# Kernel tuning notes

Measured on AMD Instinct MI355X. Metric: run time of the kernel, lower is better.

Reference implementation:

```python
import jax, jax.numpy as jnp
import numpy as np

D_MODEL = 1024
N_HEADS = 16
D_K = D_MODEL // N_HEADS
LN_EPS = 1e-5
NEG = -1e9


def setup_inputs() -> dict:
    key = jax.random.key(0)
    ks = jax.random.split(key, 12)
    B, S = 4, 2048
    s = 1.0 / np.sqrt(D_MODEL)
    # causal mask (1 = keep, 0 = masked)
    causal = jnp.tril(jnp.ones((S, S), dtype=jnp.int32))
    mask = jnp.broadcast_to(causal[None, None], (B, 1, S, S))
    return {
        "Q": jax.random.normal(ks[0], (B, S, D_MODEL), jnp.float32),
        "K": jax.random.normal(ks[1], (B, S, D_MODEL), jnp.float32),
        "V": jax.random.normal(ks[2], (B, S, D_MODEL), jnp.float32),
        "mask": mask,
        "Wq": jax.random.normal(ks[3], (D_MODEL, D_MODEL), jnp.float32) * s,
        "bq": jnp.zeros((D_MODEL,), jnp.float32),
        "Wk": jax.random.normal(ks[4], (D_MODEL, D_MODEL), jnp.float32) * s,
        "bk": jnp.zeros((D_MODEL,), jnp.float32),
        "Wv": jax.random.normal(ks[5], (D_MODEL, D_MODEL), jnp.float32) * s,
        "bv": jnp.zeros((D_MODEL,), jnp.float32),
        "Wo": jax.random.normal(ks[6], (D_MODEL, D_MODEL), jnp.float32) * s,
        "bo": jnp.zeros((D_MODEL,), jnp.float32),
        "ln_gamma": jnp.ones((D_MODEL,), jnp.float32),
        "ln_beta": jnp.zeros((D_MODEL,), jnp.float32),
    }


def _split_heads(x, B, S):
    # (B,S,D) -> (B,H,S,d_k)
    return x.reshape(B, S, N_HEADS, D_K).transpose(0, 2, 1, 3)


def reference(Q, K, V, mask, Wq, bq, Wk, bk, Wv, bv, Wo, bo, ln_gamma, ln_beta):
    B, S, _ = Q.shape
    residual = Q
    q = _split_heads(Q @ Wq + bq, B, S)
    k = _split_heads(K @ Wk + bk, B, S)
    v = _split_heads(V @ Wv + bv, B, S)
    scores = jnp.einsum("bhqd,bhkd->bhqk", q, k) / np.sqrt(D_K).astype(np.float32)
    scores = jnp.where(mask == 0, jnp.float32(NEG), scores)
    attn = jax.nn.softmax(scores, axis=-1)  # dropout p=0 -> identity
    ctx = jnp.einsum("bhqk,bhkd->bhqd", attn, v)
    ctx = ctx.transpose(0, 2, 1, 3).reshape(B, S, D_MODEL)
    out = ctx @ Wo + bo
    x = out + residual
    mu = jnp.mean(x, axis=-1, keepdims=True)
    var = jnp.mean(jnp.square(x - mu), axis=-1, keepdims=True)
    y = (x - mu) * jax.lax.rsqrt(var + LN_EPS) * ln_gamma + ln_beta
    return (y, attn)
```

## Files before the change

### kernel.cpp

```cpp
#include <hip/hip_runtime.h>

#define D_MODEL 1024
#define NH 16
#define DKH 64
#define SEQ 2048
#define BATCH 4
#define ROWS (BATCH*SEQ)

typedef _Float16 f16;
typedef _Float16 f16x4 __attribute__((ext_vector_type(4)));
typedef _Float16 f16x8 __attribute__((ext_vector_type(8)));
typedef float f32x4 __attribute__((ext_vector_type(4)));

#define MFMA16(a,b,c) __builtin_amdgcn_mfma_f32_16x16x32_f16((a),(b),(c),0,0,0)
#define CFENCE() asm volatile("" ::: "memory")

__device__ __forceinline__ void gload16(const void* g, void* l) {
  __builtin_amdgcn_global_load_lds((const __attribute__((address_space(1))) void*)g,
                                   (__attribute__((address_space(3))) void*)l,
                                   16, 0, 0);
}


__global__ __launch_bounds__(256) void cvt_w_kernel(const float* __restrict__ Wq,
    const float* __restrict__ Wk, const float* __restrict__ Wv, const float* __restrict__ Wo,
    f16* __restrict__ dst)
{
  const float* W = (blockIdx.z==0)?Wq:(blockIdx.z==1)?Wk:(blockIdx.z==2)?Wv:Wo;
  f16* d = dst + (size_t)blockIdx.z * ((size_t)D_MODEL*D_MODEL);
  int idx = blockIdx.x*256 + threadIdx.x;
  int k = idx>>10, n = idx&1023;
  d[(size_t)n*D_MODEL + k] = (f16)W[idx];
}


template<int AF32>
__global__ __launch_bounds__(256) void gemm128(
    const void* __restrict__ A0, const void* __restrict__ A1, const void* __restrict__ A2,
    const f16* __restrict__ WTbase,
    const float* __restrict__ bias0, const float* __restrict__ bias1, const float* __restrict__ bias2,
    f16* __restrict__ out0, f16* __restrict__ out1, f16* __restrict__ out2,
    const float* __restrict__ resid, float* __restrict__ xout, int modeBase)
{
  __shared__ f16 Al[2][128*32];
  __shared__ f16 Bl[2][128*32];
  const int t = threadIdx.x, w = t>>6, l = t&63;
  const int nwg = (int)gridDim.x;
  const int wg = ((int)blockIdx.x & 7) * (nwg >> 3) + ((int)blockIdx.x >> 3);
  const int z  = wg >> 9;
  const int r2 = wg & 511;
  const int bm = r2 >> 3, bn = r2 & 7;
  const int mode = modeBase + z;
  const f16* WT = WTbase + (size_t)mode * ((size_t)D_MODEL*D_MODEL);
  const float* bias = (mode==0)?bias0:(mode==1)?bias1:(mode==2)?bias2:bias0;
  const int wm = w>>1, wn = w&1;
  const int lr = l>>2, lc = l&3, fr = l&15, fg = l>>4;
  f32x4 acc[4][4] = {};
  const char* Bb = (const char*)(WT + (size_t)bn*128*D_MODEL);

#define STAGEB(bufv, ktv) do { \
    char* Bd = (char*)&Bl[0][0] + (bufv)*8192; \
    _Pragma("unroll") \
    for (int cc=0; cc<2; ++cc) { \
      int r0 = w*32 + cc*16; \
      gload16(Bb + (size_t)(r0+lr)*2048 + (ktv)*64 + lc*16, Bd + r0*64); \
    } \
  } while(0)

#define COMPUTEK(bufv) do { \
    const f16* Ac = (const f16*)((char*)&Al[0][0] + (bufv)*8192); \
    const f16* Bc = (const f16*)((char*)&Bl[0][0] + (bufv)*8192); \
    f16x8 a[4], b[4]; \
    _Pragma("unroll") \
    for (int i=0;i<4;++i) a[i] = *(const f16x8*)(Ac + (wm*64+i*16+fr)*32 + fg*8); \
    _Pragma("unroll") \
    for (int j=0;j<4;++j) b[j] = *(const f16x8*)(Bc + (wn*64+j*16+fr)*32 + fg*8); \
    _Pragma("unroll") \
    for (int i=0;i<4;++i) \
      _Pragma("unroll") \
      for (int j=0;j<4;++j) \
        acc[i][j] = MFMA16(a[i], b[j], acc[i][j]); \
  } while(0)

#define LOADA_TO(dst, ktv) do { \
    _Pragma("unroll") \
    for (int s=0;s<2;++s) \
      _Pragma("unroll") \
      for (int q=0;q<2;++q) \
        dst[s][q] = *(const f32x4*)(Arow + (size_t)s*16*1024 + (ktv)*32 + q*4); \
  } while(0)

#define WRITEA_FROM(src, bufv) do { \
    char* Ad = (char*)&Al[0][0] + (bufv)*8192 + w*2048 + l*16; \
    _Pragma("unroll") \
    for (int s=0;s<2;++s) { \
      f16x8 pk; \
      _Pragma("unroll") \
      for (int q=0;q<2;++q) \
        _Pragma("unroll") \
        for (int m2=0;m2<4;++m2) pk[q*4+m2] = (f16)src[s][q][m2]; \
      *(f16x8*)(Ad + s*1024) = pk; \
    } \
  } while(0)

#define BAR_FENCED() do { __builtin_amdgcn_s_barrier(); CFENCE(); } while(0)

  if constexpr (AF32) {
    const float* A32 = (const float*)((z==0)?A0:(z==1)?A1:A2);
    const float* Arow = A32 + (size_t)(bm*128 + w*32 + (l>>2))*1024 + (l&3)*8;
    f32x4 laA[2][2], laB[2][2];
    LOADA_TO(laA, 0);
    STAGEB(0, 0);
    WRITEA_FROM(laA, 0);
    LOADA_TO(laB, 1);
    CFENCE();
    for (int kt2=0; kt2<30; kt2+=2) {
      STAGEB((kt2+1)&1, kt2+1);
      LOADA_TO(laA, kt2+2);
      asm volatile("s_waitcnt vmcnt(6) lgkmcnt(0)" ::: "memory");
      BAR_FENCED();
      COMPUTEK(kt2&1);
      WRITEA_FROM(laB, (kt2+1)&1);
      CFENCE();
      BAR_FENCED();
      STAGEB((kt2+2)&1, kt2+2);
      LOADA_TO(laB, kt2+3);
      asm volatile("s_waitcnt vmcnt(6) lgkmcnt(0)" ::: "memory");
      BAR_FENCED();
      COMPUTEK((kt2+1)&1);
      WRITEA_FROM(laA, (kt2+2)&1);
      CFENCE();
      BAR_FENCED();
    }
    STAGEB(1, 31);
    asm volatile("s_waitcnt vmcnt(6) lgkmcnt(0)" ::: "memory");
    BAR_FENCED();
    COMPUTEK(0);
    WRITEA_FROM(laB, 1);
    CFENCE();
    BAR_FENCED();
    asm volatile("s_waitcnt vmcnt(0) lgkmcnt(0)" ::: "memory");
    BAR_FENCED();
    COMPUTEK(1);
  } else {
    const char* Ab = (const char*)((const f16*)A0 + (size_t)bm*128*D_MODEL);
    auto STAGEA = [&](int bufv, int ktv) {
      char* Ad = (char*)&Al[0][0] + bufv*8192;
      #pragma unroll
      for (int cc=0; cc<2; ++cc) {
        int r0 = w*32 + cc*16;
        gload16(Ab + (size_t)(r0+lr)*2048 + ktv*64 + lc*16, Ad + r0*64);
      }
    };
    STAGEA(0,0); STAGEB(0, 0);
    CFENCE();
    for (int kt=0; kt<31; ++kt) {
      const int cur = kt & 1;
      STAGEA(cur^1, kt+1);
      STAGEB(cur^1, kt+1);
      asm volatile("s_waitcnt vmcnt(4)" ::: "memory");
      BAR_FENCED();
      COMPUTEK(cur);
      CFENCE();
      BAR_FENCED();
    }
    asm volatile("s_waitcnt vmcnt(0)" ::: "memory");
    BAR_FENCED();
    COMPUTEK(1);
  }

#undef STAGEB
#undef COMPUTEK
#undef LOADA_TO
#undef WRITEA_FROM
#undef BAR_FENCED

  #pragma unroll
  for (int j=0;j<4;++j) {
    int col = bn*128 + wn*64 + j*16 + fr;
    float bz = bias[col];
    #pragma unroll
    for (int i=0;i<4;++i) {
      int row0 = bm*128 + wm*64 + i*16 + fg*4;
      f32x4 v = acc[i][j];
      if (mode==0) {
        int hh = col>>6, dk = col&63;
        #pragma unroll
        for (int r=0;r<4;++r) {
          int row = row0+r; int b_ = row>>11, s = row&(SEQ-1);
          out0[((size_t)(b_*NH+hh)*SEQ + s)*DKH + dk] = (f16)((v[r]+bz)*0.125f);
        }
      } else if (mode==1) {
        int hh = col>>6, dk = col&63;
        #pragma unroll
        for (int r=0;r<4;++r) {
          int row = row0+r; int b_ = row>>11, s = row&(SEQ-1);
          out1[((size_t)(b_*NH+hh)*SEQ + s)*DKH + dk] = (f16)(v[r]+bz);
        }
      } else if (mode==2) {
        int hh = col>>6, dk = col&63;
        int b_ = row0>>11, s0 = row0&(SEQ-1);
        f16x4 pk;
        #pragma unroll
        for (int r=0;r<4;++r) pk[r] = (f16)(v[r]+bz);
        *(f16x4*)(out2 + ((size_t)(b_*NH+hh)*DKH + dk)*SEQ + s0) = pk;
      } else {
        #pragma unroll
        for (int r=0;r<4;++r) {
          size_t o = (size_t)(row0+r)*D_MODEL + col;
          xout[o] = v[r] + bz + resid[o];
        }
      }
    }
  }
}


__global__ __launch_bounds__(256) void attn_kernel(
    const f16* __restrict__ qws, const f16* __restrict__ kws, const f16* __restrict__ vTws,
    float* __restrict__ attn, f16* __restrict__ ctx)
{
  __shared__ f16 el[4][32*128];
  const int t = threadIdx.x, w = t>>6, l = t&63;
  const int wg = ((int)blockIdx.x & 7)*64 + ((int)blockIdx.x >> 3);
  const int bh = wg >> 3;
  const int pr = wg & 7;
  const int qtA = pr, qtB = 15 - pr;
  const int fr = l & 15, fg = l >> 4;
  const f16* kp = kws + (size_t)bh*SEQ*DKH;
  const f16* vp = vTws + (size_t)bh*DKH*SEQ;
  const f16* qpA = qws + ((size_t)bh*SEQ + (size_t)qtA*128)*DKH;
  const f16* qpB = qws + ((size_t)bh*SEQ + (size_t)qtB*128)*DKH;
  float* apA = attn + ((size_t)bh*SEQ + (size_t)qtA*128)*SEQ;
  float* apB = attn + ((size_t)bh*SEQ + (size_t)qtB*128)*SEQ;
  f16* elw = (f16*)&el[w][0];
  const int swzx = (fr & 7) << 2;
  const int rbrow = l >> 5;
  const int rbslot = l & 31;

  f16x8 qfA[2][2], qfB[2][2];
  #pragma unroll
  for (int i=0;i<2;++i)
    #pragma unroll
    for (int kc=0;kc<2;++kc) {
      qfA[i][kc] = *(const f16x8*)(qpA + (w*32 + i*16 + fr)*DKH + kc*32 + fg*8);
      qfB[i][kc] = *(const f16x8*)(qpB + (w*32 + i*16 + fr)*DKH + kc*32 + fg*8);
    }

  auto fill_tile = [&](float* apr, int kt2) {
    f32x4 z4 = {0.f,0.f,0.f,0.f};
    #pragma unroll
    for (int i2=0;i2<16;++i2) {
      int idx = t + i2*256;
      int row = idx >> 5, c4 = idx & 31;
      __builtin_nontemporal_store(z4, (f32x4*)(apr + (size_t)row*SEQ + (size_t)kt2*128 + c4*4));
    }
  };
  const int cB = pr;

  float psumA[2] = {0.f,0.f}, psumB[2] = {0.f,0.f};
  int u = 0, f = 0;
  const int np1 = qtB + 1;
  auto drip_fills = [&]() {
    while (f*np1 < u*15) {
      if (f < cB) fill_tile(apB, qtB+1+f);
      else        fill_tile(apA, qtA+1+(f-cB));
      ++f;
    }
  };

  for (int kt=0; kt<=qtA; ++kt) {
    const f16* kb = kp + (size_t)kt*128*DKH;
    const bool diagA = (kt == qtA);
    #pragma unroll
    for (int jh=0; jh<2; ++jh) {
      f32x4 scB[2][4] = {};
      f32x4 scA[2][4] = {};
      #pragma unroll
      for (int j2=0;j2<4;++j2) {
        const int j = jh*4 + j2;
        #pragma unroll
        for (int kc=0;kc<2;++kc) {
          f16x8 kf = *(const f16x8*)(kb + (j*16+fr)*DKH + kc*32 + fg*8);
          scB[0][j2] = MFMA16(kf, qfB[0][kc], scB[0][j2]);
          scB[1][j2] = MFMA16(kf, qfB[1][kc], scB[1][j2]);
          scA[0][j2] = MFMA16(kf, qfA[0][kc], scA[0][j2]);
          scA[1][j2] = MFMA16(kf, qfA[1][kc], scA[1][j2]);
        }
      }
      #pragma unroll
      for (int i=0;i<2;++i)
        #pragma unroll
        for (int j2=0;j2<4;++j2)
          #pragma unroll
          for (int r=0;r<4;++r) psumB[i] += __expf(scB[i][j2][r]);
      if (diagA) {
        #pragma unroll
        for (int i=0;i<2;++i) {
          int rloc = w*32 + i*16 + fr;
          #pragma unroll
          for (int j2=0;j2<4;++j2)
            #pragma unroll
            for (int r=0;r<4;++r) {
              int cloc = (jh*4+j2)*16 + fg*4 + r;
              if (cloc <= rloc) psumA[i] += __expf(scA[i][j2][r]);
            }
        }
      } else {
        #pragma unroll
        for (int i=0;i<2;++i)
          #pragma unroll
          for (int j2=0;j2<4;++j2)
            #pragma unroll
            for (int r=0;r<4;++r) psumA[i] += __expf(scA[i][j2][r]);
      }
    }
    ++u; drip_fills();
  }

  for (int kt=qtA+1; kt<=qtB; ++kt) {
    const f16* kb = kp + (size_t)kt*128*DKH;
    const bool diagB = (kt == qtB);
    #pragma unroll
    for (int jh=0; jh<2; ++jh) {
      f32x4 sc[2][4] = {};
      #pragma unroll
      for (int j2=0;j2<4;++j2) {
        const int j = jh*4 + j2;
        #pragma unroll
        for (int kc=0;kc<2;++kc) {
          f16x8 kf = *(const f16x8*)(kb + (j*16+fr)*DKH + kc*32 + fg*8);
          sc[0][j2] = MFMA16(kf, qfB[0][kc], sc[0][j2]);
          sc[1][j2] = MFMA16(kf, qfB[1][kc], sc[1][j2]);
        }
      }
      if (diagB) {
        #pragma unroll
        for (int i=0;i<2;++i) {
          int rloc = w*32 + i*16 + fr;
          #pragma unroll
          for (int j2=0;j2<4;++j2)
            #pragma unroll
            for (int r=0;r<4;++r) {
              int cloc = (jh*4+j2)*16 + fg*4 + r;
              if (cloc <= rloc) psumB[i] += __expf(sc[i][j2][r]);
            }
        }
      } else {
        #pragma unroll
        for (int i=0;i<2;++i)
          #pragma unroll
          for (int j2=0;j2<4;++j2)
            #pragma unroll
            for (int r=0;r<4;++r) psumB[i] += __expf(sc[i][j2][r]);
      }
    }
    ++u; drip_fills();
  }

  #pragma unroll
  for (int m=16; m<64; m<<=1) {
    psumA[0] += __shfl_xor(psumA[0], m, 64);
    psumA[1] += __shfl_xor(psumA[1], m, 64);
    psumB[0] += __shfl_xor(psumB[0], m, 64);
    psumB[1] += __shfl_xor(psumB[1], m, 64);
  }
  float rinvA[2] = {1.f/psumA[0], 1.f/psumA[1]};
  float rinvB[2] = {1.f/psumB[0], 1.f/psumB[1]};

  f32x4 av[2][4];
  auto pass2_tile = [&](int ktv, bool diag, const f16x8 (&qf)[2][2], const float (&rinv)[2], float* apr) {
    const f16* kb = kp + (size_t)ktv*128*DKH;
    #pragma unroll
    for (int jh=0; jh<2; ++jh) {
      f32x4 sc[2][4] = {};
      __builtin_amdgcn_s_setprio(1);
      #pragma unroll
      for (int j2=0;j2<4;++j2) {
        const int j = jh*4 + j2;
        #pragma unroll
        for (int kc=0;kc<2;++kc) {
          f16x8 kf = *(const f16x8*)(kb + (j*16+fr)*DKH + kc*32 + fg*8);
          sc[0][j2] = MFMA16(kf, qf[0][kc], sc[0][j2]);
          sc[1][j2] = MFMA16(kf, qf[1][kc], sc[1][j2]);
        }
      }
      __builtin_amdgcn_s_setprio(0);
      #pragma unroll
      for (int i=0;i<2;++i) {
        const int rloc = w*32 + i*16 + fr;
        #pragma unroll
        for (int j2=0;j2<4;++j2) {
          const int j = jh*4 + j2;
          f16x4 ef;
          #pragma unroll
          for (int r=0;r<4;++r) {
            int cloc = j*16 + fg*4 + r;
            float e = (diag && cloc > rloc) ? 0.f : __expf(sc[i][j2][r]) * rinv[i];
            ef[r] = (f16)e;
          }
          *(f16x4*)(elw + (i*16+fr)*128 + (((j*4+fg) ^ swzx) << 2)) = ef;
        }
      }
    }
    {
      float* apk = apr + (size_t)(w*32)*SEQ + (size_t)ktv*128;
      #pragma unroll
      for (int p=0;p<16;++p) {
        int row = p*2 + rbrow;
        f16x4 pv4 = *(const f16x4*)(elw + row*128 + ((rbslot ^ ((row&7)<<2)) << 2));
        f32x4 o4; o4[0]=(float)pv4[0]; o4[1]=(float)pv4[1]; o4[2]=(float)pv4[2]; o4[3]=(float)pv4[3];
        __builtin_nontemporal_store(o4, (f32x4*)(apk + (size_t)row*SEQ + rbslot*4));
      }
    }
    __builtin_amdgcn_s_setprio(1);
    #pragma unroll
    for (int c=0;c<4;++c) {
      f16x8 pf0 = *(const f16x8*)(elw + (fr)*128    + (((c*8+fg*2) ^ swzx) << 2));
      f16x8 pf1 = *(const f16x8*)(elw + (16+fr)*128 + (((c*8+fg*2) ^ swzx) << 2));
      #pragma unroll
      for (int j2=0;j2<4;++j2) {
        f16x8 vf = *(const f16x8*)(vp + (j2*16+fr)*SEQ + ktv*128 + c*32 + fg*8);
        av[0][j2] = MFMA16(vf, pf0, av[0][j2]);
        av[1][j2] = MFMA16(vf, pf1, av[1][j2]);
      }
    }
    __builtin_amdgcn_s_setprio(0);
  };
  auto ctx_store = [&](int qtv) {
    const int b_ = bh >> 4, hh = bh & 15;
    #pragma unroll
    for (int i=0;i<2;++i) {
      size_t rowoff = ((size_t)b_*SEQ + (size_t)qtv*128 + w*32 + i*16 + fr) * D_MODEL + hh*DKH;
      #pragma unroll
      for (int j2=0;j2<4;++j2) {
        f16x4 pk;
        #pragma unroll
        for (int r=0;r<4;++r) pk[r] = (f16)av[i][j2][r];
        *(f16x4*)(ctx + rowoff + j2*16 + fg*4) = pk;
      }
    }
  };

  #pragma unroll
  for (int i=0;i<2;++i)
    #pragma unroll
    for (int j2=0;j2<4;++j2) av[i][j2] = (f32x4){0.f,0.f,0.f,0.f};
  for (int kt=0; kt<=qtA; ++kt) pass2_tile(kt, kt==qtA, qfA, rinvA, apA);
  ctx_store(qtA);

  #pragma unroll
  for (int i=0;i<2;++i)
    #pragma unroll
    for (int j2=0;j2<4;++j2) av[i][j2] = (f32x4){0.f,0.f,0.f,0.f};
  for (int kt=0; kt<=qtB; ++kt) pass2_tile(kt, kt==qtB, qfB, rinvB, apB);
  ctx_store(qtB);
}


__global__ __launch_bounds__(256) void ln_kernel(const float* __restrict__ x,
    const float* __restrict__ gamma, const float* __restrict__ beta, float* __restrict__ y)
{
  __shared__ float red[4];
  __shared__ float red2[4];
  const int t = threadIdx.x, w = t>>6, l = t&63;
  const size_t row = blockIdx.x;
  float4 v = ((const float4*)(x + row*D_MODEL))[t];
  float s = v.x+v.y+v.z+v.w;
  #pragma unroll
  for (int m=1;m<64;m<<=1) s += __shfl_xor(s, m, 64);
  if (l==0) red[w] = s;
  __syncthreads();
  float mu = (red[0]+red[1]+red[2]+red[3]) * (1.f/D_MODEL);
  float dx=v.x-mu, dy=v.y-mu, dz=v.z-mu, dw=v.w-mu;
  float q = dx*dx+dy*dy+dz*dz+dw*dw;
  #pragma unroll
  for (int m=1;m<64;m<<=1) q += __shfl_xor(q, m, 64);
  if (l==0) red2[w] = q;
  __syncthreads();
  float var = (red2[0]+red2[1]+red2[2]+red2[3]) * (1.f/D_MODEL);
  float rs = rsqrtf(var + 1e-5f);
  float4 g  = ((const float4*)gamma)[t];
  float4 bb = ((const float4*)beta)[t];
  float4 o;
  o.x = dx*rs*g.x + bb.x;
  o.y = dy*rs*g.y + bb.y;
  o.z = dz*rs*g.z + bb.z;
  o.w = dw*rs*g.w + bb.w;
  ((float4*)(y + row*D_MODEL))[t] = o;
}


extern "C" void kernel_launch(void* const* d_in, const int* in_sizes, int n_in,
                              void* d_out, int out_size, void* d_ws, size_t ws_size,
                              hipStream_t stream)
{
  const float* Q  = (const float*)d_in[0];
  const float* K  = (const float*)d_in[1];
  const float* V  = (const float*)d_in[2];
  const float* Wq = (const float*)d_in[4];
  const float* bq = (const float*)d_in[5];
  const float* Wk = (const float*)d_in[6];
  const float* bk = (const float*)d_in[7];
  const float* Wv = (const float*)d_in[8];
  const float* bv = (const float*)d_in[9];
  const float* Wo = (const float*)d_in[10];
  const float* bo = (const float*)d_in[11];
  const float* gam= (const float*)d_in[12];
  const float* bet= (const float*)d_in[13];

  float* y    = (float*)d_out;
  float* attn = y + (size_t)ROWS*D_MODEL;

  char* ws = (char*)d_ws;
  const size_t SZ = (size_t)ROWS*D_MODEL*sizeof(f16);
  f16* ctx   = (f16*)ws;
  float* xb  = (float*)(ws + SZ);
  f16* WT    = (f16*)(ws + 3*SZ);
  f16* qws   = (f16*)(ws + 3*SZ + ((size_t)4*D_MODEL*D_MODEL*sizeof(f16)));
  f16* kws   = (f16*)((char*)qws + SZ);
  f16* vT    = (f16*)((char*)kws + SZ);

  cvt_w_kernel<<<dim3(4096,1,4), 256, 0, stream>>>(Wq, Wk, Wv, Wo, WT);
  gemm128<1><<<1536, 256, 0, stream>>>(Q, K, V, WT, bq, bk, bv, qws, kws, vT, nullptr, nullptr, 0);
  attn_kernel<<<512, 256, 0, stream>>>(qws, kws, vT, attn, ctx);
  gemm128<0><<<512, 256, 0, stream>>>(ctx, nullptr, nullptr, WT, bo, bo, bo, nullptr, nullptr, nullptr, Q, xb, 3);
  ln_kernel<<<8192, 256, 0, stream>>>(xb, gam, bet, y);
}
```

Baseline: 465.6 us.

## Stage fp32 A tiles via direct LDS loads with swizzle; triple-buffer fp16 GEMM

In the fp32-input GEMM path, A tiles are now fetched straight into LDS as fp32 using global_load_lds with an XOR swizzle. They are converted to fp16 at fragment-read time, replacing the register load, convert and LDS write path. The fp16-input path gains a three-stage LDS ring buffer, so loads are issued two tiles ahead. The aim is to cut VGPR staging and expose more load latency overlap, at the cost of more LDS (48KB), which may reduce occupancy, plus extra conversion work inside the compute loop.

Measured after the change: 451.6 us. 1.03x faster.

```diff
diff --git a/kernel.cpp b/kernel.cpp
--- a/kernel.cpp
+++ b/kernel.cpp
@@ -42,8 +42,7 @@
     f16* __restrict__ out0, f16* __restrict__ out1, f16* __restrict__ out2,
     const float* __restrict__ resid, float* __restrict__ xout, int modeBase)
 {
-  __shared__ f16 Al[2][128*32];
-  __shared__ f16 Bl[2][128*32];
+  __shared__ __align__(128) char ldsb[49152];
   const int t = threadIdx.x, w = t>>6, l = t&63;
   const int nwg = (int)gridDim.x;
   const int wg = ((int)blockIdx.x & 7) * (nwg >> 3) + ((int)blockIdx.x >> 3);
@@ -58,8 +57,23 @@
   f32x4 acc[4][4] = {};
   const char* Bb = (const char*)(WT + (size_t)bn*128*D_MODEL);
 
-#define STAGEB(bufv, ktv) do { \
-    char* Bd = (char*)&Bl[0][0] + (bufv)*8192; \
+#define BAR_FENCED() do { __builtin_amdgcn_s_barrier(); CFENCE(); } while(0)
+
+  if constexpr (AF32) {
+    const float* A32 = (const float*)((z==0)?A0:(z==1)?A1:A2);
+    const char* Ag = (const char*)A32 + ((size_t)(bm*128 + (t>>3)) * 4096)
+                     + (size_t)(((t&7) ^ ((t>>3)&7)) << 4);
+    const int su0 = (((fg*2)   ^ (fr&7)) << 4);
+    const int su1 = (((fg*2+1) ^ (fr&7)) << 4);
+
+#define STAGEA32(bufv, ktv) do { \
+    _Pragma("unroll") \
+    for (int cc=0; cc<4; ++cc) \
+      gload16(Ag + (size_t)cc*131072 + (size_t)(ktv)*128, ldsb + (bufv)*16384 + cc*4096 + t*16); \
+  } while(0)
+
+#define STAGEB32(bufv, ktv) do { \
+    char* Bd = ldsb + 32768 + (bufv)*8192; \
     _Pragma("unroll") \
     for (int cc=0; cc<2; ++cc) { \
       int r0 = w*32 + cc*16; \
@@ -67,12 +81,20 @@
     } \
   } while(0)
 
-#define COMPUTEK(bufv) do { \
-    const f16* Ac = (const f16*)((char*)&Al[0][0] + (bufv)*8192); \
-    const f16* Bc = (const f16*)((char*)&Bl[0][0] + (bufv)*8192); \
+#define COMPUTE32(bufv) do { \
+    const char* Abl = ldsb + (bufv)*16384; \
+    const f16* Bc = (const f16*)(ldsb + 32768 + (bufv)*8192); \
     f16x8 a[4], b[4]; \
     _Pragma("unroll") \
-    for (int i=0;i<4;++i) a[i] = *(const f16x8*)(Ac + (wm*64+i*16+fr)*32 + fg*8); \
+    for (int i=0;i<4;++i) { \
+      const char* rb = Abl + (wm*64 + i*16 + fr)*128; \
+      f32x4 lo = *(const f32x4*)(rb + su0); \
+      f32x4 hi = *(const f32x4*)(rb + su1); \
+      f16x8 t8; \
+      _Pragma("unroll") \
+      for (int m2=0;m2<4;++m2) { t8[m2] = (f16)lo[m2]; t8[4+m2] = (f16)hi[m2]; } \
+      a[i] = t8; \
+    } \
     _Pragma("unroll") \
     for (int j=0;j<4;++j) b[j] = *(const f16x8*)(Bc + (wn*64+j*16+fr)*32 + fg*8); \
     _Pragma("unroll") \
@@ -82,97 +104,77 @@
         acc[i][j] = MFMA16(a[i], b[j], acc[i][j]); \
   } while(0)
 
-#define LOADA_TO(dst, ktv) do { \
-    _Pragma("unroll") \
-    for (int s=0;s<2;++s) \
-      _Pragma("unroll") \
-      for (int q=0;q<2;++q) \
-        dst[s][q] = *(const f32x4*)(Arow + (size_t)s*16*1024 + (ktv)*32 + q*4); \
-  } while(0)
-
-#define WRITEA_FROM(src, bufv) do { \
-    char* Ad = (char*)&Al[0][0] + (bufv)*8192 + w*2048 + l*16; \
-    _Pragma("unroll") \
-    for (int s=0;s<2;++s) { \
-      f16x8 pk; \
-      _Pragma("unroll") \
-      for (int q=0;q<2;++q) \
-        _Pragma("unroll") \
-        for (int m2=0;m2<4;++m2) pk[q*4+m2] = (f16)src[s][q][m2]; \
-      *(f16x8*)(Ad + s*1024) = pk; \
-    } \
-  } while(0)
-
-#define BAR_FENCED() do { __builtin_amdgcn_s_barrier(); CFENCE(); } while(0)
-
-  if constexpr (AF32) {
-    const float* A32 = (const float*)((z==0)?A0:(z==1)?A1:A2);
-    const float* Arow = A32 + (size_t)(bm*128 + w*32 + (l>>2))*1024 + (l&3)*8;
-    f32x4 laA[2][2], laB[2][2];
-    LOADA_TO(laA, 0);
-    STAGEB(0, 0);
-    WRITEA_FROM(laA, 0);
-    LOADA_TO(laB, 1);
-    CFENCE();
-    for (int kt2=0; kt2<30; kt2+=2) {
-      STAGEB((kt2+1)&1, kt2+1);
-      LOADA_TO(laA, kt2+2);
-      asm volatile("s_waitcnt vmcnt(6) lgkmcnt(0)" ::: "memory");
-      BAR_FENCED();
-      COMPUTEK(kt2&1);
-      WRITEA_FROM(laB, (kt2+1)&1);
-      CFENCE();
-      BAR_FENCED();
-      STAGEB((kt2+2)&1, kt2+2);
-      LOADA_TO(laB, kt2+3);
-      asm volatile("s_waitcnt vmcnt(6) lgkmcnt(0)" ::: "memory");
-      BAR_FENCED();
-      COMPUTEK((kt2+1)&1);
-      WRITEA_FROM(laA, (kt2+2)&1);
-      CFENCE();
-      BAR_FENCED();
-    }
-    STAGEB(1, 31);
-    asm volatile("s_waitcnt vmcnt(6) lgkmcnt(0)" ::: "memory");
-    BAR_FENCED();
-    COMPUTEK(0);
-    WRITEA_FROM(laB, 1);
-    CFENCE();
-    BAR_FENCED();
-    asm volatile("s_waitcnt vmcnt(0) lgkmcnt(0)" ::: "memory");
-    BAR_FENCED();
-    COMPUTEK(1);
-  } else {
-    const char* Ab = (const char*)((const f16*)A0 + (size_t)bm*128*D_MODEL);
-    auto STAGEA = [&](int bufv, int ktv) {
-      char* Ad = (char*)&Al[0][0] + bufv*8192;
-      #pragma unroll
-      for (int cc=0; cc<2; ++cc) {
-        int r0 = w*32 + cc*16;
-        gload16(Ab + (size_t)(r0+lr)*2048 + ktv*64 + lc*16, Ad + r0*64);
-      }
-    };
-    STAGEA(0,0); STAGEB(0, 0);
+    STAGEA32(0, 0); STAGEB32(0, 0);
     CFENCE();
     for (int kt=0; kt<31; ++kt) {
       const int cur = kt & 1;
-      STAGEA(cur^1, kt+1);
-      STAGEB(cur^1, kt+1);
-      asm volatile("s_waitcnt vmcnt(4)" ::: "memory");
+      STAGEA32(cur^1, kt+1);
+      STAGEB32(cur^1, kt+1);
+      asm volatile("s_waitcnt vmcnt(6)" ::: "memory");
       BAR_FENCED();
-      COMPUTEK(cur);
+      COMPUTE32(cur);
       CFENCE();
       BAR_FENCED();
     }
     asm volatile("s_waitcnt vmcnt(0)" ::: "memory");
     BAR_FENCED();
-    COMPUTEK(1);
+    COMPUTE32(1);
+
+#undef STAGEA32
+#undef STAGEB32
+#undef COMPUTE32
+  } else {
+    const char* Ab = (const char*)((const f16*)A0 + (size_t)bm*128*D_MODEL);
+
+#define STAGE16(bufv, ktv) do { \
+    char* Ad = ldsb + (bufv)*8192; \
+    char* Bd = ldsb + 24576 + (bufv)*8192; \
+    _Pragma("unroll") \
+    for (int cc=0; cc<2; ++cc) { \
+      int r0 = w*32 + cc*16; \
+      gload16(Ab + (size_t)(r0+lr)*2048 + (ktv)*64 + lc*16, Ad + r0*64); \
+      gload16(Bb + (size_t)(r0+lr)*2048 + (ktv)*64 + lc*16, Bd + r0*64); \
+    } \
+  } while(0)
+
+#define COMPUTE16(bufv) do { \
+    const f16* Ac = (const f16*)(ldsb + (bufv)*8192); \
+    const f16* Bc = (const f16*)(ldsb + 24576 + (bufv)*8192); \
+    f16x8 a[4], b[4]; \
+    _Pragma("unroll") \
+    for (int i=0;i<4;++i) a[i] = *(const f16x8*)(Ac + (wm*64+i*16+fr)*32 + fg*8); \
+    _Pragma("unroll") \
+    for (int j=0;j<4;++j) b[j] = *(const f16x8*)(Bc + (wn*64+j*16+fr)*32 + fg*8); \
+    _Pragma("unroll") \
+    for (int i=0;i<4;++i) \
+      _Pragma("unroll") \
+      for (int j=0;j<4;++j) \
+        acc[i][j] = MFMA16(a[i], b[j], acc[i][j]); \
+  } while(0)
+
+    STAGE16(0, 0); STAGE16(1, 1);
+    CFENCE();
+    for (int kt=0; kt<30; ++kt) {
+      STAGE16((kt+2)%3, kt+2);
+      asm volatile("s_waitcnt vmcnt(8)" ::: "memory");
+      BAR_FENCED();
+      COMPUTE16(kt%3);
+      CFENCE();
+      BAR_FENCED();
+    }
+    asm volatile("s_waitcnt vmcnt(4)" ::: "memory");
+    BAR_FENCED();
+    COMPUTE16(0);
+    CFENCE();
+    BAR_FENCED();
+    asm volatile("s_waitcnt vmcnt(0)" ::: "memory");
+    BAR_FENCED();
+    COMPUTE16(1);
+
+#undef STAGE16
+#undef COMPUTE16
   }
 
-#undef STAGEB
-#undef COMPUTEK
-#undef LOADA_TO
-#undef WRITEA_FROM
 #undef BAR_FENCED
 
   #pragma unroll
```
